# Performance work log

Hardware: AMD Instinct MI355X
Metric: run time of the kernel (lower is better)

The kernel has to match this reference:

```python
import jax, jax.numpy as jnp
import numpy as np

B, M = 4, 4096          # events x points-per-event (row_splits are uniform)
N = B * M
IN_DIM, SPACE, PROP, K = 128, 4, 64, 32


def setup_inputs() -> dict:
    key = jax.random.key(0)
    k1, k2, k3, k4, k5 = jax.random.split(key, 5)
    x = jax.random.normal(k1, (N, IN_DIM), jnp.float32)
    row_splits = (jnp.arange(B + 1, dtype=jnp.int32) * M)
    s = 1.0 / np.sqrt(IN_DIM)
    Ws = jax.random.uniform(k2, (IN_DIM, SPACE), jnp.float32, -s, s)
    bs = jax.random.uniform(k3, (SPACE,), jnp.float32, -s, s)
    Wp = jax.random.uniform(k4, (IN_DIM, PROP), jnp.float32, -s, s)
    bp = jax.random.uniform(k5, (PROP,), jnp.float32, -s, s)
    return {"x": x, "Ws": Ws, "bs": bs, "Wp": Wp, "bp": bp, "row_splits": row_splits}


def _gravnet(x, Ws, bs, Wp, bp):
    space = x @ Ws + bs                      # [N, SPACE] learned coordinates
    prop = x @ Wp + bp                       # [N, PROP]  features to propagate
    sp = space.reshape(B, M, SPACE)
    pr = prop.reshape(B, M, PROP)
    # exact KNN within each event (row_splits segment): pairwise squared dists
    sq = jnp.sum(sp * sp, axis=-1)                         # [B, M]
    d2 = sq[:, :, None] + sq[:, None, :] - 2.0 * jnp.einsum("bms,bns->bmn", sp, sp)
    neg_vals, idx = jax.lax.top_k(-d2, K)                  # k smallest dists (incl. self)
    distsq = jnp.maximum(-neg_vals, 0.0)                   # [B, M, K]
    weights = jnp.exp(-10.0 * distsq)                      # [B, M, K]
    gathered = jax.vmap(lambda p, i: p[i])(pr, idx)        # [B, M, K, PROP]
    weighted = gathered * weights[..., None]
    fmean = jnp.mean(weighted, axis=2)                     # [B, M, PROP]
    fmax = jnp.max(weighted, axis=2)                       # [B, M, PROP]
    out = jnp.concatenate([fmean, fmax], axis=-1)          # [B, M, 2*PROP]
    return out.reshape(N, 2 * PROP)


def reference(x, Ws, bs, Wp, bp, row_splits):
    # row_splits encodes uniform segments [0, M, 2M, ...]; KNN never crosses them.
    return _gravnet(x, Ws, bs, Wp, bp)
```

## Files before the change

### kernel.cpp

```cpp
#include <hip/hip_runtime.h>
#include <hip/hip_bf16.h>
#include <math.h>

#define N_TOT   16384
#define M_EV    4096
#define IN_DIM  128
#define SPACE_D 4
#define PROP_D  64
#define K_NN    32
#define CAND_CAP 128
#define MARGIN  0.04f

typedef _Float16 h2 __attribute__((ext_vector_type(2)));
typedef unsigned long long u64;

__device__ __forceinline__ h2 pkmin(h2 a, h2 b) {
#if __has_builtin(__builtin_elementwise_min)
  return __builtin_elementwise_min(a, b);
#else
  h2 r; r.x = (a.x < b.x) ? a.x : b.x; r.y = (a.y < b.y) ? a.y : b.y; return r;
#endif
}

__device__ __forceinline__ h2 pkrtz(float a, float b) {
  return __builtin_bit_cast(h2, __builtin_amdgcn_cvt_pkrtz(a, b));
}

__global__ __launch_bounds__(256) void linear_kernel(
    const float* __restrict__ x,
    const float* __restrict__ Ws, const float* __restrict__ bs,
    const float* __restrict__ Wp, const float* __restrict__ bp,
    float* __restrict__ space, float* __restrict__ prop)
{
  const int lane = threadIdx.x & 63;
  const int wid  = threadIdx.x >> 6;
  const int r0   = __builtin_amdgcn_readfirstlane((int)blockIdx.x * 16 + wid * 4);

  const float* xr = x + (size_t)r0 * IN_DIM;

  float a0 = bp[lane];
  float a1 = a0, a2 = a0, a3 = a0;
  #pragma unroll
  for (int i = 0; i < IN_DIM; ++i) {
    const float w = Wp[i * PROP_D + lane];
    a0 = fmaf(xr[i],              w, a0);
    a1 = fmaf(xr[IN_DIM + i],     w, a1);
    a2 = fmaf(xr[2 * IN_DIM + i], w, a2);
    a3 = fmaf(xr[3 * IN_DIM + i], w, a3);
  }
  prop[(size_t)(r0 + 0) * PROP_D + lane] = a0;
  prop[(size_t)(r0 + 1) * PROP_D + lane] = a1;
  prop[(size_t)(r0 + 2) * PROP_D + lane] = a2;
  prop[(size_t)(r0 + 3) * PROP_D + lane] = a3;

  if (lane < 16) {
    const int r = lane >> 2, c = lane & 3;
    const float* xq = x + (size_t)(r0 + r) * IN_DIM;
    float a = bs[c];
    #pragma unroll
    for (int i = 0; i < IN_DIM; ++i)
      a = fmaf(xq[i], Ws[i * SPACE_D + c], a);
    space[(size_t)(r0 + r) * SPACE_D + c] = a;
  }
}

__device__ __forceinline__ int mbcnt64(u64 mk) {
  return (int)__builtin_amdgcn_mbcnt_hi((unsigned)(mk >> 32),
           __builtin_amdgcn_mbcnt_lo((unsigned)mk, 0u));
}

__global__ __launch_bounds__(512, 8) void knn_kernel(
    const float4* __restrict__ space,
    const float*  __restrict__ prop,
    float*        __restrict__ out)
{
  const int lane = threadIdx.x & 63;
  const int wid  = threadIdx.x >> 6;
  const int row  = (int)blockIdx.x * 8 + wid;
  const int m0   = row & ~(M_EV - 1);
  const int mloc = row & (M_EV - 1);

  __shared__ uint4 s_pk[M_EV / 2];
  __shared__ int   s_ci[8][CAND_CAP];
  __shared__ uint2 s_w[8][K_NN];
  __shared__ int   s_cnt[8];

  {
    const float4* src = space + m0;
    #pragma unroll
    for (int it = 0; it < 4; ++it) {
      const int i = (int)threadIdx.x + it * 512;
      const float4 a = src[i];
      const float4 b = src[i + 2048];
      s_pk[i] = make_uint4(
        __builtin_bit_cast(unsigned, pkrtz(a.x, b.x)),
        __builtin_bit_cast(unsigned, pkrtz(a.y, b.y)),
        __builtin_bit_cast(unsigned, pkrtz(a.z, b.z)),
        __builtin_bit_cast(unsigned, pkrtz(a.w, b.w)));
    }
  }
  if (lane == 0) s_cnt[wid] = 0;
  __syncthreads();

  const float4 qf = space[m0 + mloc];
  const h2 qx = pkrtz(qf.x, qf.x), qy = pkrtz(qf.y, qf.y);
  const h2 qz = pkrtz(qf.z, qf.z), qw = pkrtz(qf.w, qf.w);

  unsigned pd[32];
  h2 mn; mn.x = (_Float16)65504.f; mn.y = (_Float16)65504.f;
  #pragma unroll
  for (int t = 0; t < 32; ++t) {
    const uint4 u = s_pk[lane + (t << 6)];
    const h2 dx = qx - __builtin_bit_cast(h2, u.x);
    const h2 dy = qy - __builtin_bit_cast(h2, u.y);
    const h2 dz = qz - __builtin_bit_cast(h2, u.z);
    const h2 dw = qw - __builtin_bit_cast(h2, u.w);
    h2 s = dx * dx;
    s = dy * dy + s;
    s = dz * dz + s;
    s = dw * dw + s;
    pd[t] = __builtin_bit_cast(unsigned, s);
    mn = pkmin(mn, s);
  }

  const unsigned mnbits = __builtin_bit_cast(unsigned, mn);
  const unsigned c0 = mnbits & 0xFFFFu, c1 = mnbits >> 16;
  unsigned blo = 0u, bhi = 0x7C00u;
  while (blo < bhi) {
    const unsigned mid = (blo + bhi) >> 1;
    const int c = (int)__popcll(__ballot(c0 <= mid)) +
                  (int)__popcll(__ballot(c1 <= mid));
    if (c >= K_NN) { bhi = mid; if (c == K_NN) break; }
    else blo = mid + 1;
  }
  const float T = (float)__builtin_bit_cast(_Float16, (unsigned short)bhi) + MARGIN;
  const h2 Th = pkrtz(T, T);

  #pragma unroll
  for (int t = 0; t < 32; ++t) asm volatile("" : "+v"(pd[t]));

  #pragma unroll
  for (int t = 0; t < 32; ++t) {
    const h2 s = __builtin_bit_cast(h2, pd[t]);
    if (s.x <= Th.x) {
      const int pos = atomicAdd(&s_cnt[wid], 1);
      if (pos < CAND_CAP) s_ci[wid][pos] = (t << 6) + lane;
    }
    if (s.y <= Th.y) {
      const int pos = atomicAdd(&s_cnt[wid], 1);
      if (pos < CAND_CAP) s_ci[wid][pos] = (t << 6) + lane + 2048;
    }
  }
  int C = s_cnt[wid];

  if (C > CAND_CAP) {
    const float4* __restrict__ ev = space + m0;
    unsigned lo = 0u, hi = __float_as_uint(T);
    while (lo < hi) {
      const unsigned mid = (lo + hi) >> 1;
      const float fm = __uint_as_float(mid);
      int c = 0;
      #pragma unroll 1
      for (int t = 0; t < 64; ++t) {
        const float4 cc = ev[lane + (t << 6)];
        const float dx = qf.x - cc.x, dy = qf.y - cc.y;
        const float dz = qf.z - cc.z, dw = qf.w - cc.w;
        const float dd = fmaf(dx, dx, fmaf(dy, dy, fmaf(dz, dz, dw * dw)));
        c += (int)__popcll(__ballot(dd <= fm));
      }
      if (c >= K_NN) { hi = mid; if (c == K_NN) break; }
      else lo = mid + 1;
    }
    const float Tf = __uint_as_float(hi);
    int cnt = 0;
    #pragma unroll 1
    for (int pass = 0; pass < 2; ++pass) {
      #pragma unroll 1
      for (int t = 0; t < 64; ++t) {
        const float4 cc = ev[lane + (t << 6)];
        const float dx = qf.x - cc.x, dy = qf.y - cc.y;
        const float dz = qf.z - cc.z, dw = qf.w - cc.w;
        const float dd = fmaf(dx, dx, fmaf(dy, dy, fmaf(dz, dz, dw * dw)));
        const bool p = pass ? (dd == Tf) : (dd < Tf);
        const u64 mk = __ballot(p);
        if (p) {
          const int pos = cnt + mbcnt64(mk);
          if (pos < K_NN) s_ci[wid][pos] = (t << 6) + lane;
        }
        cnt += (int)__popcll(mk);
      }
      if (cnt >= K_NN) break;
    }
    C = K_NN;
  }

  const bool h0 = (lane < C), h1 = (64 + lane < C);
  const int i0 = h0 ? s_ci[wid][lane]      : 0;
  const int i1 = h1 ? s_ci[wid][64 + lane] : 0;
  float v0 = INFINITY, v1 = INFINITY;
  if (h0) {
    const float4 cc = space[m0 + i0];
    const float dx = qf.x - cc.x, dy = qf.y - cc.y;
    const float dz = qf.z - cc.z, dw = qf.w - cc.w;
    v0 = fmaf(dx, dx, fmaf(dy, dy, fmaf(dz, dz, dw * dw)));
  }
  if (h1) {
    const float4 cc = space[m0 + i1];
    const float dx = qf.x - cc.x, dy = qf.y - cc.y;
    const float dz = qf.z - cc.z, dw = qf.w - cc.w;
    v1 = fmaf(dx, dx, fmaf(dy, dy, fmaf(dz, dz, dw * dw)));
  }

  unsigned lo = 0u, hi = __float_as_uint(T);
  while (lo < hi) {
    const unsigned mid = (lo + hi) >> 1;
    const float fm = __uint_as_float(mid);
    const int c = (int)__popcll(__ballot(v0 <= fm)) +
                  (int)__popcll(__ballot(v1 <= fm));
    if (c >= K_NN) { hi = mid; if (c == K_NN) break; }
    else lo = mid + 1;
  }
  const float T2 = __uint_as_float(hi);

  const u64 mkE0 = __ballot(v0 == T2);
  const u64 mkE1 = __ballot(v1 == T2);
  const int L = (int)__popcll(__ballot(v0 < T2)) +
                (int)__popcll(__ballot(v1 < T2));
  const int e = K_NN - L;
  const int nE0 = (int)__popcll(mkE0);
  const bool sel0 = (v0 < T2) || ((v0 == T2) && (mbcnt64(mkE0) < e));
  const bool sel1 = (v1 < T2) || ((v1 == T2) && (nE0 + mbcnt64(mkE1) < e));

  const float w0 = __expf(-10.f * v0);
  const float w1 = __expf(-10.f * v1);

  {
    const u64 mkS0 = __ballot(sel0);
    if (sel0) {
      const int pos = mbcnt64(mkS0);
      s_w[wid][pos] = make_uint2((unsigned)i0, __float_as_uint(w0));
    }
    const int b0 = (int)__popcll(mkS0);
    const u64 mkS1 = __ballot(sel1);
    if (sel1) {
      const int pos = b0 + mbcnt64(mkS1);
      s_w[wid][pos] = make_uint2((unsigned)i1, __float_as_uint(w1));
    }
  }

  float accm = 0.f;
  float accx = -INFINITY;
  const float* __restrict__ pb = prop + ((size_t)m0 << 6) + lane;
  #pragma unroll 8
  for (int n = 0; n < K_NN; ++n) {
    const uint2 wn = s_w[wid][n];
    const float w = __uint_as_float(wn.y);
    const float v = pb[(size_t)wn.x << 6];
    const float wv = w * v;
    accm += wv;
    accx = fmaxf(accx, wv);
  }
  out[(size_t)row * 128 + lane]      = accm * (1.f / K_NN);
  out[(size_t)row * 128 + 64 + lane] = accx;
}

extern "C" void kernel_launch(void* const* d_in, const int* in_sizes, int n_in,
                              void* d_out, int out_size, void* d_ws, size_t ws_size,
                              hipStream_t stream) {
  const float* x  = (const float*)d_in[0];
  const float* Ws = (const float*)d_in[1];
  const float* bs = (const float*)d_in[2];
  const float* Wp = (const float*)d_in[3];
  const float* bp = (const float*)d_in[4];
  float* out = (float*)d_out;

  float* prop  = (float*)d_ws;
  float* space = (float*)((char*)d_ws + (size_t)N_TOT * PROP_D * sizeof(float));

  linear_kernel<<<N_TOT / 16, 256, 0, stream>>>(x, Ws, bs, Wp, bp, space, prop);
  knn_kernel<<<N_TOT / 8, 512, 0, stream>>>((const float4*)space, prop, out);
}
```

Before: 52.99 us.

## Vectorize linear kernel x loads, relax knn launch bounds, loosen register barrier

The linear kernel now reads each input row as float4 instead of scalar floats. Because the row address is wave-uniform, the compiler can issue wider scalar or vector loads. The knn kernel's launch_bounds minimum-blocks hint drops from 8 to 6, giving the compiler more registers per thread at the cost of possible occupancy. The per-register asm barrier that pinned the packed distance values is replaced by a single memory clobber, which gives the scheduler more freedom but may let it rematerialize or spill values differently.

```diff
diff --git a/kernel.cpp b/kernel.cpp
--- a/kernel.cpp
+++ b/kernel.cpp
@@ -36,17 +36,24 @@
   const int wid  = threadIdx.x >> 6;
   const int r0   = __builtin_amdgcn_readfirstlane((int)blockIdx.x * 16 + wid * 4);
 
-  const float* xr = x + (size_t)r0 * IN_DIM;
+  const float4* __restrict__ xr = (const float4*)(x + (size_t)r0 * IN_DIM);
 
   float a0 = bp[lane];
   float a1 = a0, a2 = a0, a3 = a0;
   #pragma unroll
-  for (int i = 0; i < IN_DIM; ++i) {
-    const float w = Wp[i * PROP_D + lane];
-    a0 = fmaf(xr[i],              w, a0);
-    a1 = fmaf(xr[IN_DIM + i],     w, a1);
-    a2 = fmaf(xr[2 * IN_DIM + i], w, a2);
-    a3 = fmaf(xr[3 * IN_DIM + i], w, a3);
+  for (int i = 0; i < 32; ++i) {
+    const float4 x0 = xr[i];
+    const float4 x1 = xr[32 + i];
+    const float4 x2 = xr[64 + i];
+    const float4 x3 = xr[96 + i];
+    #pragma unroll
+    for (int d = 0; d < 4; ++d) {
+      const float w = Wp[(i * 4 + d) * PROP_D + lane];
+      a0 = fmaf(((const float*)&x0)[d], w, a0);
+      a1 = fmaf(((const float*)&x1)[d], w, a1);
+      a2 = fmaf(((const float*)&x2)[d], w, a2);
+      a3 = fmaf(((const float*)&x3)[d], w, a3);
+    }
   }
   prop[(size_t)(r0 + 0) * PROP_D + lane] = a0;
   prop[(size_t)(r0 + 1) * PROP_D + lane] = a1;
@@ -55,11 +62,16 @@
 
   if (lane < 16) {
     const int r = lane >> 2, c = lane & 3;
-    const float* xq = x + (size_t)(r0 + r) * IN_DIM;
+    const float4* __restrict__ xq = (const float4*)(x + (size_t)(r0 + r) * IN_DIM);
     float a = bs[c];
     #pragma unroll
-    for (int i = 0; i < IN_DIM; ++i)
-      a = fmaf(xq[i], Ws[i * SPACE_D + c], a);
+    for (int i = 0; i < 32; ++i) {
+      const float4 v = xq[i];
+      a = fmaf(v.x, Ws[(i * 4 + 0) * SPACE_D + c], a);
+      a = fmaf(v.y, Ws[(i * 4 + 1) * SPACE_D + c], a);
+      a = fmaf(v.z, Ws[(i * 4 + 2) * SPACE_D + c], a);
+      a = fmaf(v.w, Ws[(i * 4 + 3) * SPACE_D + c], a);
+    }
     space[(size_t)(r0 + r) * SPACE_D + c] = a;
   }
 }
@@ -69,7 +81,7 @@
            __builtin_amdgcn_mbcnt_lo((unsigned)mk, 0u));
 }
 
-__global__ __launch_bounds__(512, 8) void knn_kernel(
+__global__ __launch_bounds__(512, 6) void knn_kernel(
     const float4* __restrict__ space,
     const float*  __restrict__ prop,
     float*        __restrict__ out)
@@ -136,8 +148,7 @@
   const float T = (float)__builtin_bit_cast(_Float16, (unsigned short)bhi) + MARGIN;
   const h2 Th = pkrtz(T, T);
 
-  #pragma unroll
-  for (int t = 0; t < 32; ++t) asm volatile("" : "+v"(pd[t]));
+  asm volatile("" ::: "memory");
 
   #pragma unroll
   for (int t = 0; t < 32; ++t) {
```

After: 53.37 us. No clear change (+0.7%).
